# Optimization experiments

Measured on AMD Instinct MI355X. Metric: run time of the kernel, lower is better.

Reference implementation:

```python
import jax, jax.numpy as jnp
import numpy as np
from jax import lax

# Mamba hyperparams implied by Mamba(d_model=8, d_state=16, d_conv=4, expand=2)
D_MODEL, D_STATE, D_CONV, EXPAND = 8, 16, 4, 2
D_INNER = EXPAND * D_MODEL          # 16
DT_RANK = -(-D_MODEL // 16)          # ceil(8/16) = 1
BATCH, SEQ_LEN, NUM_CLASSES = 1024, 250, 12


def silu(v):
    return v * jax.nn.sigmoid(v)


def setup_inputs() -> dict:
    key = jax.random.key(0)
    ks = jax.random.split(key, 12)
    s = 0.05
    return {
        "x": jax.random.normal(ks[0], (BATCH, D_MODEL, SEQ_LEN), jnp.float32),
        "in_proj_w": jax.random.normal(ks[1], (2 * D_INNER, D_MODEL), jnp.float32) * s,
        "conv_w": jax.random.normal(ks[2], (D_INNER, D_CONV), jnp.float32) * s,
        "conv_b": jax.random.normal(ks[3], (D_INNER,), jnp.float32) * s,
        "x_proj_w": jax.random.normal(ks[4], (DT_RANK + 2 * D_STATE, D_INNER), jnp.float32) * s,
        "dt_proj_w": jax.random.normal(ks[5], (D_INNER, DT_RANK), jnp.float32) * s,
        "dt_proj_b": jax.random.normal(ks[6], (D_INNER,), jnp.float32) * s,
        "A_log": jnp.log(jnp.tile(jnp.arange(1, D_STATE + 1, dtype=jnp.float32), (D_INNER, 1))),
        "D": jnp.ones((D_INNER,), jnp.float32),
        "out_proj_w": jax.random.normal(ks[7], (D_MODEL, D_INNER), jnp.float32) * s,
        "fc_w": jax.random.normal(ks[8], (NUM_CLASSES, D_MODEL * SEQ_LEN), jnp.float32) * s,
        "fc_b": jax.random.normal(ks[9], (NUM_CLASSES,), jnp.float32) * s,
    }


def reference(x, in_proj_w, conv_w, conv_b, x_proj_w, dt_proj_w, dt_proj_b,
              A_log, D, out_proj_w, fc_w, fc_b):
    B = x.shape[0]
    xt = jnp.transpose(x, (0, 2, 1))                       # (B, L, d_model)
    xz = xt @ in_proj_w.T                                  # (B, L, 2*d_inner)
    x_in, z = xz[..., :D_INNER], xz[..., D_INNER:]

    # causal depthwise conv1d along time, kernel d_conv, padding d_conv-1, crop to L
    xp = jnp.pad(x_in, ((0, 0), (D_CONV - 1, 0), (0, 0)))  # (B, L+3, d_inner)
    acc = conv_b
    for k in range(D_CONV):  # small fixed kernel loop
        acc = acc + conv_w[:, k] * xp[:, k:k + SEQ_LEN, :]
    u = silu(acc)                                          # (B, L, d_inner)

    x_dbl = u @ x_proj_w.T                                 # (B, L, dt_rank+2*d_state)
    dt = x_dbl[..., :DT_RANK]
    Bm = x_dbl[..., DT_RANK:DT_RANK + D_STATE]             # (B, L, d_state)
    Cm = x_dbl[..., DT_RANK + D_STATE:]                    # (B, L, d_state)
    delta = jax.nn.softplus(dt @ dt_proj_w.T + dt_proj_b)  # (B, L, d_inner)

    A = -jnp.exp(A_log)                                    # (d_inner, d_state)
    dA = jnp.exp(delta[..., None] * A)                     # (B, L, d_inner, d_state)
    dBu = delta[..., None] * Bm[:, :, None, :] * u[..., None]

    def step(h, inp):
        dA_t, dBu_t, C_t = inp
        h = dA_t * h + dBu_t                               # (B, d_inner, d_state)
        y_t = jnp.einsum('bds,bs->bd', h, C_t)
        return h, y_t

    h0 = jnp.zeros((B, D_INNER, D_STATE), x.dtype)
    _, ys = lax.scan(step, h0, (jnp.moveaxis(dA, 1, 0),
                                jnp.moveaxis(dBu, 1, 0),
                                jnp.moveaxis(Cm, 1, 0)))
    y = jnp.moveaxis(ys, 0, 1) + u * D                     # (B, L, d_inner)
    y = y * silu(z)
    out = y @ out_proj_w.T                                 # (B, L, d_model)

    flat = out.reshape(B, D_MODEL * SEQ_LEN)
    return flat @ fc_w.T + fc_b                            # (B, num_classes)
```

## Files before the change

### kernel.cpp

```cpp
#include <hip/hip_runtime.h>
#include <hip/hip_fp16.h>
#include <math.h>

#define SEQ 250
#define ST  252
#define NCLS 12

typedef __attribute__((ext_vector_type(4))) _Float16 half4v;
typedef __attribute__((ext_vector_type(4))) float    float4v;

template<int CTRL>
__device__ __forceinline__ float dpp_add(float v) {
    int t = __builtin_amdgcn_update_dpp(0, __float_as_int(v), CTRL, 0xF, 0xF, true);
    return v + __int_as_float(t);
}

__device__ __forceinline__ __half2 f_as_h2(float f) {
    union { float f; __half2 h; } u; u.f = f; return u.h;
}
__device__ __forceinline__ float h2_as_f(__half2 h) {
    union { __half2 h; float f; } u; u.h = h; return u.f;
}

__global__ __launch_bounds__(512)
void mamba_cls_kernel(
    const float* __restrict__ x,
    const float* __restrict__ in_proj_w,
    const float* __restrict__ conv_w,
    const float* __restrict__ conv_b,
    const float* __restrict__ x_proj_w,
    const float* __restrict__ dt_proj_w,
    const float* __restrict__ dt_proj_b,
    const float* __restrict__ A_log,
    const float* __restrict__ Dp,
    const float* __restrict__ out_proj_w,
    const float* __restrict__ fc_w,
    const float* __restrict__ fc_b,
    float* __restrict__ out)
{
    __shared__ __align__(16) __half2 s_bc [2][16 * ST];
    __shared__ __align__(16) __half2 s_dlu[2][16 * ST];
    __shared__ __align__(16) __half  s_sz [2][16 * ST];

    const int tid  = threadIdx.x;
    const int p    = tid >> 8;
    const int tid8 = tid & 255;
    const int b0   = blockIdx.x * 2;

    {
        float4* s_xf4 = (float4*)s_dlu[0];
        const float4* __restrict__ xb4 =
            (const float4*)(x + (size_t)b0 * (8 * SEQ));
        for (int i = tid; i < 1000; i += 512) s_xf4[i] = xb4[i];
    }
    __syncthreads();

    {
        float* s_f  = (float*)s_bc[p];
        const float* s_xf = (const float*)s_dlu[0] + p * (8 * SEQ);
        const int d  = tid8 & 15;
        const int t0 = tid8 >> 4;
        float w1[8], w2[8];
        #pragma unroll
        for (int m = 0; m < 8; ++m) {
            w1[m] = in_proj_w[d * 8 + m];
            w2[m] = in_proj_w[(16 + d) * 8 + m];
        }
        #pragma unroll
        for (int i = 0; i < 16; ++i) {
            int t = t0 + i * 16;
            if (t < SEQ) {
                float acc = 0.f, z = 0.f;
                #pragma unroll
                for (int m = 0; m < 8; ++m) {
                    float xv = s_xf[m * SEQ + t];
                    acc = fmaf(w1[m], xv, acc);
                    z   = fmaf(w2[m], xv, z);
                }
                s_f[d * ST + t] = acc;
                s_sz[p][d * ST + t] = __float2half(z / (1.f + __expf(-z)));
            }
        }
    }
    __syncthreads();

    {
        const float* s_f = (const float*)s_bc[p];
        const int d  = tid8 & 15;
        const int t0 = tid8 >> 4;
        float cw[4];
        #pragma unroll
        for (int k = 0; k < 4; ++k) cw[k] = conv_w[d * 4 + k];
        const float cb = conv_b[d];
        #pragma unroll
        for (int i = 0; i < 16; ++i) {
            int t = t0 + i * 16;
            if (t < SEQ) {
                float acc = cb;
                #pragma unroll
                for (int k = 0; k < 4; ++k) {
                    int tt = t + k - 3;
                    if (tt >= 0) acc = fmaf(cw[k], s_f[d * ST + tt], acc);
                }
                float sg = 1.f / (1.f + __expf(-acc));
                s_dlu[p][d * ST + t].y = __float2half(acc * sg);
            }
        }
    }
    __syncthreads();

    {
        const int wave = tid8 >> 6;
        const int l    = tid8 & 63;
        const int rowc = l & 15;
        const int kg   = l >> 4;

        half4v wB, wC, wD;
        #pragma unroll
        for (int i = 0; i < 4; ++i) {
            wB[i] = (_Float16)x_proj_w[(1  + rowc) * 16 + 4 * kg + i];
            wC[i] = (_Float16)x_proj_w[(17 + rowc) * 16 + 4 * kg + i];
            wD[i] = (_Float16)x_proj_w[4 * kg + i];
        }
        const float dtw_c = dt_proj_w[rowc];
        const float dtb_c = dt_proj_b[rowc];
        const float4v zero4 = {0.f, 0.f, 0.f, 0.f};
        const unsigned int* __restrict__ dlu_w = (const unsigned int*)s_dlu[p];

        for (int tile = wave; tile < 16; tile += 4) {
            const int t0 = tile * 16;
            unsigned int w0 = dlu_w[(4 * kg + 0) * ST + t0 + rowc];
            unsigned int w1 = dlu_w[(4 * kg + 1) * ST + t0 + rowc];
            unsigned int w2 = dlu_w[(4 * kg + 2) * ST + t0 + rowc];
            unsigned int w3 = dlu_w[(4 * kg + 3) * ST + t0 + rowc];
            union { unsigned int u[2]; half4v h; } A;
            A.u[0] = (w0 >> 16) | (w1 & 0xFFFF0000u);
            A.u[1] = (w2 >> 16) | (w3 & 0xFFFF0000u);

            float4v dB = __builtin_amdgcn_mfma_f32_16x16x16f16(A.h, wB, zero4, 0, 0, 0);
            float4v dC = __builtin_amdgcn_mfma_f32_16x16x16f16(A.h, wC, zero4, 0, 0, 0);
            float4v dT = __builtin_amdgcn_mfma_f32_16x16x16f16(A.h, wD, zero4, 0, 0, 0);

            const int tb = t0 + kg * 4;
            if (tb <= 248) {
                __half2 h0 = __floats2half2_rn(dB[0], dC[0]);
                __half2 h1 = __floats2half2_rn(dB[1], dC[1]);
                __half2 h2 = __floats2half2_rn(dB[2], dC[2]);
                __half2 h3 = __floats2half2_rn(dB[3], dC[3]);
                float4 wv;
                wv.x = h2_as_f(h0); wv.y = h2_as_f(h1);
                wv.z = h2_as_f(h2); wv.w = h2_as_f(h3);
                *reinterpret_cast<float4*>(s_bc[p] + rowc * ST + tb) = wv;
            }
            #pragma unroll
            for (int r = 0; r < 4; ++r) {
                int t = tb + r;
                if (t < SEQ) {
                    float v  = fmaf(dT[r], dtw_c, dtb_c);
                    float dl = (v > 20.f) ? v : __logf(1.f + __expf(v));
                    s_dlu[p][rowc * ST + t].x = __float2half(dl);
                }
            }
        }
    }
    __syncthreads();

    if (tid < 256) {
        const int sp   = tid >> 7;
        const int i7   = tid & 127;
        const int d    = i7 >> 3;
        const int s2   = i7 & 7;
        const float A2a = -__expf(A_log[d * 16 + s2])     * 1.4426950408889634f;
        const float A2b = -__expf(A_log[d * 16 + s2 + 8]) * 1.4426950408889634f;
        const float Dd  = Dp[d];
        const __half2* __restrict__ dlu_p = s_dlu[sp] + d * ST;
        const __half2* __restrict__ bca_p = s_bc [sp] + s2 * ST;
        const __half2* __restrict__ bcb_p = s_bc [sp] + (s2 + 8) * ST;
        const __half*  __restrict__ sz_p  = (const __half*)s_sz[sp] + d * ST;
        float* __restrict__ y_p = (float*)s_dlu[sp] + d * ST;
        float ha = 0.f, hb = 0.f;
        for (int t = 0; t < 248; t += 8) {
            float4 du_a = *reinterpret_cast<const float4*>(dlu_p + t);
            float4 du_b = *reinterpret_cast<const float4*>(dlu_p + t + 4);
            float4 ba_a = *reinterpret_cast<const float4*>(bca_p + t);
            float4 ba_b = *reinterpret_cast<const float4*>(bca_p + t + 4);
            float4 bb_a = *reinterpret_cast<const float4*>(bcb_p + t);
            float4 bb_b = *reinterpret_cast<const float4*>(bcb_p + t + 4);
            float2 sza  = *reinterpret_cast<const float2*>(sz_p + t);
            float2 szb  = *reinterpret_cast<const float2*>(sz_p + t + 4);

            float fdu[8] = {du_a.x, du_a.y, du_a.z, du_a.w,
                            du_b.x, du_b.y, du_b.z, du_b.w};
            float fba[8] = {ba_a.x, ba_a.y, ba_a.z, ba_a.w,
                            ba_b.x, ba_b.y, ba_b.z, ba_b.w};
            float fbb[8] = {bb_a.x, bb_a.y, bb_a.z, bb_a.w,
                            bb_b.x, bb_b.y, bb_b.z, bb_b.w};
            float2 s0 = __half22float2(f_as_h2(sza.x));
            float2 s1 = __half22float2(f_as_h2(sza.y));
            float2 s2f = __half22float2(f_as_h2(szb.x));
            float2 s3 = __half22float2(f_as_h2(szb.y));
            float fsz[8] = {s0.x, s0.y, s1.x, s1.y, s2f.x, s2f.y, s3.x, s3.y};

            float yv[8];
            #pragma unroll
            for (int tt = 0; tt < 8; ++tt) {
                float2 du  = __half22float2(f_as_h2(fdu[tt]));
                float2 bca = __half22float2(f_as_h2(fba[tt]));
                float2 bcb = __half22float2(f_as_h2(fbb[tt]));
                float dlu = du.x * du.y;
                ha = fmaf(exp2f(du.x * A2a), ha, dlu * bca.x);
                hb = fmaf(exp2f(du.x * A2b), hb, dlu * bcb.x);
                float r = fmaf(hb, bcb.y, ha * bca.y);
                r = dpp_add<0xB1>(r);
                r = dpp_add<0x4E>(r);
                r = dpp_add<0x141>(r);
                yv[tt] = fmaf(du.y, Dd, r) * fsz[tt];
            }
            if (s2 == 0) {
                float4 y4;
                y4.x = yv[0]; y4.y = yv[1]; y4.z = yv[2]; y4.w = yv[3];
                *reinterpret_cast<float4*>(y_p + t) = y4;
                y4.x = yv[4]; y4.y = yv[5]; y4.z = yv[6]; y4.w = yv[7];
                *reinterpret_cast<float4*>(y_p + t + 4) = y4;
            }
        }
        {
            float2 duv2 = *reinterpret_cast<const float2*>(dlu_p + 248);
            float2 bca2 = *reinterpret_cast<const float2*>(bca_p + 248);
            float2 bcb2 = *reinterpret_cast<const float2*>(bcb_p + 248);
            float2 szf  = __half22float2(*reinterpret_cast<const __half2*>(sz_p + 248));
            float fdu[2] = {duv2.x, duv2.y};
            float fba[2] = {bca2.x, bca2.y};
            float fbb[2] = {bcb2.x, bcb2.y};
            float fsz[2] = {szf.x, szf.y};
            float yv[2];
            #pragma unroll
            for (int tt = 0; tt < 2; ++tt) {
                float2 du  = __half22float2(f_as_h2(fdu[tt]));
                float2 bca = __half22float2(f_as_h2(fba[tt]));
                float2 bcb = __half22float2(f_as_h2(fbb[tt]));
                float dlu = du.x * du.y;
                ha = fmaf(exp2f(du.x * A2a), ha, dlu * bca.x);
                hb = fmaf(exp2f(du.x * A2b), hb, dlu * bcb.x);
                float r = fmaf(hb, bcb.y, ha * bca.y);
                r = dpp_add<0xB1>(r);
                r = dpp_add<0x4E>(r);
                r = dpp_add<0x141>(r);
                yv[tt] = fmaf(du.y, Dd, r) * fsz[tt];
            }
            if (s2 == 0) {
                float2 y2; y2.x = yv[0]; y2.y = yv[1];
                *reinterpret_cast<float2*>(y_p + 248) = y2;
            }
        }
    }
    __syncthreads();

    {
        float* s_f  = (float*)s_bc[p];
        const float* s_yf = (const float*)s_dlu[p];
        const int j = tid8 & 7;
        float w[16];
        #pragma unroll
        for (int d2 = 0; d2 < 16; ++d2) w[d2] = out_proj_w[j * 16 + d2];
        for (int t0 = (tid8 >> 3) * 4; t0 < SEQ; t0 += 128) {
            float a0 = 0.f, a1 = 0.f, a2 = 0.f, a3 = 0.f;
            #pragma unroll
            for (int d2 = 0; d2 < 16; ++d2) {
                float4 y4 = *reinterpret_cast<const float4*>(s_yf + d2 * ST + t0);
                a0 = fmaf(w[d2], y4.x, a0);
                a1 = fmaf(w[d2], y4.y, a1);
                a2 = fmaf(w[d2], y4.z, a2);
                a3 = fmaf(w[d2], y4.w, a3);
            }
            s_f[(t0 + 0) * 8 + j] = a0;
            s_f[(t0 + 1) * 8 + j] = a1;
            if (t0 + 2 < SEQ) s_f[(t0 + 2) * 8 + j] = a2;
            if (t0 + 3 < SEQ) s_f[(t0 + 3) * 8 + j] = a3;
        }
    }
    __syncthreads();

    {
        float* s_yf = (float*)s_dlu[p];
        float p_[NCLS];
        #pragma unroll
        for (int c = 0; c < NCLS; ++c) p_[c] = 0.f;
        const float4* fw4 = (const float4*)fc_w;
        const float4* sf4 = (const float4*)s_bc[p];
        for (int q = tid8; q < 500; q += 256) {
            float4 f = sf4[q];
            #pragma unroll
            for (int c = 0; c < NCLS; ++c) {
                float4 wv = fw4[c * 500 + q];
                p_[c] += f.x * wv.x + f.y * wv.y + f.z * wv.z + f.w * wv.w;
            }
        }
        #pragma unroll
        for (int c = 0; c < NCLS; ++c) {
            float v = p_[c];
            v = dpp_add<0xB1>(v);
            v = dpp_add<0x4E>(v);
            v = dpp_add<0x141>(v);
            v = dpp_add<0x140>(v);
            v += __shfl_xor(v, 16);
            v += __shfl_xor(v, 32);
            p_[c] = v;
        }
        const int wave = tid8 >> 6;
        const int lane = tid8 & 63;
        __syncthreads();
        if (lane == 0) {
            #pragma unroll
            for (int c = 0; c < NCLS; ++c) s_yf[wave * NCLS + c] = p_[c];
        }
        __syncthreads();
        if (tid8 < NCLS) {
            float v = s_yf[tid8] + s_yf[NCLS + tid8] + s_yf[2 * NCLS + tid8] +
                      s_yf[3 * NCLS + tid8] + fc_b[tid8];
            out[(size_t)(b0 + p) * NCLS + tid8] = v;
        }
    }
}

extern "C" void kernel_launch(void* const* d_in, const int* in_sizes, int n_in,
                              void* d_out, int out_size, void* d_ws, size_t ws_size,
                              hipStream_t stream) {
    const float* x          = (const float*)d_in[0];
    const float* in_proj_w  = (const float*)d_in[1];
    const float* conv_w     = (const float*)d_in[2];
    const float* conv_b     = (const float*)d_in[3];
    const float* x_proj_w   = (const float*)d_in[4];
    const float* dt_proj_w  = (const float*)d_in[5];
    const float* dt_proj_b  = (const float*)d_in[6];
    const float* A_log      = (const float*)d_in[7];
    const float* Dp         = (const float*)d_in[8];
    const float* out_proj_w = (const float*)d_in[9];
    const float* fc_w       = (const float*)d_in[10];
    const float* fc_b       = (const float*)d_in[11];
    float* out = (float*)d_out;

    const int batch = in_sizes[0] / (8 * SEQ);
    mamba_cls_kernel<<<batch / 2, 512, 0, stream>>>(
        x, in_proj_w, conv_w, conv_b, x_proj_w, dt_proj_w, dt_proj_b,
        A_log, Dp, out_proj_w, fc_w, fc_b, out);
}
```

Before: 53.42 us.

## Split selective scan into two time halves with state carry-over correction

The sequential scan over 250 steps previously used only 256 of 512 threads. Now the first half of threads scans steps 0-127 while the second half scans 128-249 from a zero state. It records the cumulative delta sum and partial output packed in fp16. A third pass then adds the carried-in state contribution, C·h127·exp(A·cumsum delta), for the second half. This halves the serial dependency chain but adds a sync, an extra correction pass, and fp16 rounding of cumulative sums and of the mid state, which risks accuracy loss.

```diff
diff --git a/kernel.cpp b/kernel.cpp
--- a/kernel.cpp
+++ b/kernel.cpp
@@ -41,6 +41,7 @@
     __shared__ __align__(16) __half2 s_bc [2][16 * ST];
     __shared__ __align__(16) __half2 s_dlu[2][16 * ST];
     __shared__ __align__(16) __half  s_sz [2][16 * ST];
+    __shared__ __half s_h127[2][256];
 
     const int tid  = threadIdx.x;
     const int p    = tid >> 8;
@@ -165,92 +166,175 @@
     }
     __syncthreads();
 
-    if (tid < 256) {
-        const int sp   = tid >> 7;
-        const int i7   = tid & 127;
-        const int d    = i7 >> 3;
-        const int s2   = i7 & 7;
+    {
+        const int sp = (tid >> 7) & 1;
+        const int i7 = tid & 127;
+        const int d  = i7 >> 3;
+        const int s2 = i7 & 7;
         const float A2a = -__expf(A_log[d * 16 + s2])     * 1.4426950408889634f;
         const float A2b = -__expf(A_log[d * 16 + s2 + 8]) * 1.4426950408889634f;
         const float Dd  = Dp[d];
         const __half2* __restrict__ dlu_p = s_dlu[sp] + d * ST;
         const __half2* __restrict__ bca_p = s_bc [sp] + s2 * ST;
         const __half2* __restrict__ bcb_p = s_bc [sp] + (s2 + 8) * ST;
-        const __half*  __restrict__ sz_p  = (const __half*)s_sz[sp] + d * ST;
         float* __restrict__ y_p = (float*)s_dlu[sp] + d * ST;
         float ha = 0.f, hb = 0.f;
-        for (int t = 0; t < 248; t += 8) {
-            float4 du_a = *reinterpret_cast<const float4*>(dlu_p + t);
-            float4 du_b = *reinterpret_cast<const float4*>(dlu_p + t + 4);
-            float4 ba_a = *reinterpret_cast<const float4*>(bca_p + t);
-            float4 ba_b = *reinterpret_cast<const float4*>(bca_p + t + 4);
-            float4 bb_a = *reinterpret_cast<const float4*>(bcb_p + t);
-            float4 bb_b = *reinterpret_cast<const float4*>(bcb_p + t + 4);
-            float2 sza  = *reinterpret_cast<const float2*>(sz_p + t);
-            float2 szb  = *reinterpret_cast<const float2*>(sz_p + t + 4);
-
-            float fdu[8] = {du_a.x, du_a.y, du_a.z, du_a.w,
-                            du_b.x, du_b.y, du_b.z, du_b.w};
-            float fba[8] = {ba_a.x, ba_a.y, ba_a.z, ba_a.w,
-                            ba_b.x, ba_b.y, ba_b.z, ba_b.w};
-            float fbb[8] = {bb_a.x, bb_a.y, bb_a.z, bb_a.w,
-                            bb_b.x, bb_b.y, bb_b.z, bb_b.w};
-            float2 s0 = __half22float2(f_as_h2(sza.x));
-            float2 s1 = __half22float2(f_as_h2(sza.y));
-            float2 s2f = __half22float2(f_as_h2(szb.x));
-            float2 s3 = __half22float2(f_as_h2(szb.y));
-            float fsz[8] = {s0.x, s0.y, s1.x, s1.y, s2f.x, s2f.y, s3.x, s3.y};
-
-            float yv[8];
-            #pragma unroll
-            for (int tt = 0; tt < 8; ++tt) {
-                float2 du  = __half22float2(f_as_h2(fdu[tt]));
-                float2 bca = __half22float2(f_as_h2(fba[tt]));
-                float2 bcb = __half22float2(f_as_h2(fbb[tt]));
-                float dlu = du.x * du.y;
-                ha = fmaf(exp2f(du.x * A2a), ha, dlu * bca.x);
-                hb = fmaf(exp2f(du.x * A2b), hb, dlu * bcb.x);
-                float r = fmaf(hb, bcb.y, ha * bca.y);
-                r = dpp_add<0xB1>(r);
-                r = dpp_add<0x4E>(r);
-                r = dpp_add<0x141>(r);
-                yv[tt] = fmaf(du.y, Dd, r) * fsz[tt];
-            }
-            if (s2 == 0) {
-                float4 y4;
-                y4.x = yv[0]; y4.y = yv[1]; y4.z = yv[2]; y4.w = yv[3];
-                *reinterpret_cast<float4*>(y_p + t) = y4;
-                y4.x = yv[4]; y4.y = yv[5]; y4.z = yv[6]; y4.w = yv[7];
-                *reinterpret_cast<float4*>(y_p + t + 4) = y4;
-            }
-        }
-        {
-            float2 duv2 = *reinterpret_cast<const float2*>(dlu_p + 248);
-            float2 bca2 = *reinterpret_cast<const float2*>(bca_p + 248);
-            float2 bcb2 = *reinterpret_cast<const float2*>(bcb_p + 248);
-            float2 szf  = __half22float2(*reinterpret_cast<const __half2*>(sz_p + 248));
-            float fdu[2] = {duv2.x, duv2.y};
-            float fba[2] = {bca2.x, bca2.y};
-            float fbb[2] = {bcb2.x, bcb2.y};
-            float fsz[2] = {szf.x, szf.y};
-            float yv[2];
-            #pragma unroll
-            for (int tt = 0; tt < 2; ++tt) {
-                float2 du  = __half22float2(f_as_h2(fdu[tt]));
-                float2 bca = __half22float2(f_as_h2(fba[tt]));
-                float2 bcb = __half22float2(f_as_h2(fbb[tt]));
-                float dlu = du.x * du.y;
-                ha = fmaf(exp2f(du.x * A2a), ha, dlu * bca.x);
-                hb = fmaf(exp2f(du.x * A2b), hb, dlu * bcb.x);
-                float r = fmaf(hb, bcb.y, ha * bca.y);
-                r = dpp_add<0xB1>(r);
-                r = dpp_add<0x4E>(r);
-                r = dpp_add<0x141>(r);
-                yv[tt] = fmaf(du.y, Dd, r) * fsz[tt];
-            }
-            if (s2 == 0) {
-                float2 y2; y2.x = yv[0]; y2.y = yv[1];
-                *reinterpret_cast<float2*>(y_p + 248) = y2;
+
+        if (tid < 256) {
+            const __half* __restrict__ sz_p = (const __half*)s_sz[sp] + d * ST;
+            for (int t = 0; t < 128; t += 8) {
+                float4 du_a = *reinterpret_cast<const float4*>(dlu_p + t);
+                float4 du_b = *reinterpret_cast<const float4*>(dlu_p + t + 4);
+                float4 ba_a = *reinterpret_cast<const float4*>(bca_p + t);
+                float4 ba_b = *reinterpret_cast<const float4*>(bca_p + t + 4);
+                float4 bb_a = *reinterpret_cast<const float4*>(bcb_p + t);
+                float4 bb_b = *reinterpret_cast<const float4*>(bcb_p + t + 4);
+                float2 sza  = *reinterpret_cast<const float2*>(sz_p + t);
+                float2 szb  = *reinterpret_cast<const float2*>(sz_p + t + 4);
+
+                float fdu[8] = {du_a.x, du_a.y, du_a.z, du_a.w,
+                                du_b.x, du_b.y, du_b.z, du_b.w};
+                float fba[8] = {ba_a.x, ba_a.y, ba_a.z, ba_a.w,
+                                ba_b.x, ba_b.y, ba_b.z, ba_b.w};
+                float fbb[8] = {bb_a.x, bb_a.y, bb_a.z, bb_a.w,
+                                bb_b.x, bb_b.y, bb_b.z, bb_b.w};
+                float2 s0 = __half22float2(f_as_h2(sza.x));
+                float2 s1 = __half22float2(f_as_h2(sza.y));
+                float2 s2f = __half22float2(f_as_h2(szb.x));
+                float2 s3 = __half22float2(f_as_h2(szb.y));
+                float fsz[8] = {s0.x, s0.y, s1.x, s1.y, s2f.x, s2f.y, s3.x, s3.y};
+
+                float yv[8];
+                #pragma unroll
+                for (int q = 0; q < 8; ++q) {
+                    float2 du  = __half22float2(f_as_h2(fdu[q]));
+                    float2 bca = __half22float2(f_as_h2(fba[q]));
+                    float2 bcb = __half22float2(f_as_h2(fbb[q]));
+                    float dlu = du.x * du.y;
+                    ha = fmaf(exp2f(du.x * A2a), ha, dlu * bca.x);
+                    hb = fmaf(exp2f(du.x * A2b), hb, dlu * bcb.x);
+                    float r = fmaf(hb, bcb.y, ha * bca.y);
+                    r = dpp_add<0xB1>(r);
+                    r = dpp_add<0x4E>(r);
+                    r = dpp_add<0x141>(r);
+                    yv[q] = fmaf(du.y, Dd, r) * fsz[q];
+                }
+                if (s2 == 0) {
+                    float4 y4;
+                    y4.x = yv[0]; y4.y = yv[1]; y4.z = yv[2]; y4.w = yv[3];
+                    *reinterpret_cast<float4*>(y_p + t) = y4;
+                    y4.x = yv[4]; y4.y = yv[5]; y4.z = yv[6]; y4.w = yv[7];
+                    *reinterpret_cast<float4*>(y_p + t + 4) = y4;
+                }
+            }
+            s_h127[sp][d * 16 + s2]     = __float2half(ha);
+            s_h127[sp][d * 16 + s2 + 8] = __float2half(hb);
+        } else {
+            float Ssum = 0.f;
+            for (int t = 128; t < 248; t += 8) {
+                float4 du_a = *reinterpret_cast<const float4*>(dlu_p + t);
+                float4 du_b = *reinterpret_cast<const float4*>(dlu_p + t + 4);
+                float4 ba_a = *reinterpret_cast<const float4*>(bca_p + t);
+                float4 ba_b = *reinterpret_cast<const float4*>(bca_p + t + 4);
+                float4 bb_a = *reinterpret_cast<const float4*>(bcb_p + t);
+                float4 bb_b = *reinterpret_cast<const float4*>(bcb_p + t + 4);
+
+                float fdu[8] = {du_a.x, du_a.y, du_a.z, du_a.w,
+                                du_b.x, du_b.y, du_b.z, du_b.w};
+                float fba[8] = {ba_a.x, ba_a.y, ba_a.z, ba_a.w,
+                                ba_b.x, ba_b.y, ba_b.z, ba_b.w};
+                float fbb[8] = {bb_a.x, bb_a.y, bb_a.z, bb_a.w,
+                                bb_b.x, bb_b.y, bb_b.z, bb_b.w};
+                float wpk[8];
+                #pragma unroll
+                for (int q = 0; q < 8; ++q) {
+                    float2 du  = __half22float2(f_as_h2(fdu[q]));
+                    float2 bca = __half22float2(f_as_h2(fba[q]));
+                    float2 bcb = __half22float2(f_as_h2(fbb[q]));
+                    Ssum += du.x;
+                    float dlu = du.x * du.y;
+                    ha = fmaf(exp2f(du.x * A2a), ha, dlu * bca.x);
+                    hb = fmaf(exp2f(du.x * A2b), hb, dlu * bcb.x);
+                    float r = fmaf(hb, bcb.y, ha * bca.y);
+                    r = dpp_add<0xB1>(r);
+                    r = dpp_add<0x4E>(r);
+                    r = dpp_add<0x141>(r);
+                    float ypart = fmaf(du.y, Dd, r);
+                    wpk[q] = h2_as_f(__floats2half2_rn(Ssum, ypart));
+                }
+                if (s2 == 0) {
+                    float4 y4;
+                    y4.x = wpk[0]; y4.y = wpk[1]; y4.z = wpk[2]; y4.w = wpk[3];
+                    *reinterpret_cast<float4*>(y_p + t) = y4;
+                    y4.x = wpk[4]; y4.y = wpk[5]; y4.z = wpk[6]; y4.w = wpk[7];
+                    *reinterpret_cast<float4*>(y_p + t + 4) = y4;
+                }
+            }
+            {
+                float2 duv2 = *reinterpret_cast<const float2*>(dlu_p + 248);
+                float2 bca2 = *reinterpret_cast<const float2*>(bca_p + 248);
+                float2 bcb2 = *reinterpret_cast<const float2*>(bcb_p + 248);
+                float fdu[2] = {duv2.x, duv2.y};
+                float fba[2] = {bca2.x, bca2.y};
+                float fbb[2] = {bcb2.x, bcb2.y};
+                float wpk[2];
+                #pragma unroll
+                for (int q = 0; q < 2; ++q) {
+                    float2 du  = __half22float2(f_as_h2(fdu[q]));
+                    float2 bca = __half22float2(f_as_h2(fba[q]));
+                    float2 bcb = __half22float2(f_as_h2(fbb[q]));
+                    Ssum += du.x;
+                    float dlu = du.x * du.y;
+                    ha = fmaf(exp2f(du.x * A2a), ha, dlu * bca.x);
+                    hb = fmaf(exp2f(du.x * A2b), hb, dlu * bcb.x);
+                    float r = fmaf(hb, bcb.y, ha * bca.y);
+                    r = dpp_add<0xB1>(r);
+                    r = dpp_add<0x4E>(r);
+                    r = dpp_add<0x141>(r);
+                    float ypart = fmaf(du.y, Dd, r);
+                    wpk[q] = h2_as_f(__floats2half2_rn(Ssum, ypart));
+                }
+                if (s2 == 0) {
+                    float2 y2; y2.x = wpk[0]; y2.y = wpk[1];
+                    *reinterpret_cast<float2*>(y_p + 248) = y2;
+                }
+            }
+        }
+    }
+    __syncthreads();
+
+    {
+        const int d = tid8 >> 4;
+        const int s = tid8 & 15;
+        const float A2 = -__expf(A_log[d * 16 + s]) * 1.4426950408889634f;
+        const float hmid = __half2float(s_h127[p][d * 16 + s]);
+        float* __restrict__ y_row = (float*)s_dlu[p] + d * ST;
+        const __half2* __restrict__ bc_row = s_bc[p] + s * ST;
+        const __half*  __restrict__ sz_row = (const __half*)s_sz[p] + d * ST;
+        for (int t = 128; t < 250; t += 2) {
+            float2 w2 = *reinterpret_cast<const float2*>(y_row + t);
+            float2 c2 = *reinterpret_cast<const float2*>(bc_row + t);
+            float  szw = *reinterpret_cast<const float*>(sz_row + t);
+            float2 szv = __half22float2(f_as_h2(szw));
+
+            float2 w0 = __half22float2(f_as_h2(w2.x));
+            float2 w1 = __half22float2(f_as_h2(w2.y));
+            float  C0 = __half22float2(f_as_h2(c2.x)).y;
+            float  C1 = __half22float2(f_as_h2(c2.y)).y;
+
+            float corr0 = C0 * hmid * exp2f(A2 * w0.x);
+            corr0 = dpp_add<0xB1>(corr0);
+            corr0 = dpp_add<0x4E>(corr0);
+            corr0 = dpp_add<0x141>(corr0);
+            corr0 = dpp_add<0x140>(corr0);
+            float corr1 = C1 * hmid * exp2f(A2 * w1.x);
+            corr1 = dpp_add<0xB1>(corr1);
+            corr1 = dpp_add<0x4E>(corr1);
+            corr1 = dpp_add<0x141>(corr1);
+            corr1 = dpp_add<0x140>(corr1);
+            if (s == 0) {
+                y_row[t]     = (w0.y + corr0) * szv.x;
+                y_row[t + 1] = (w1.y + corr1) * szv.y;
             }
         }
     }
```

After: 70.89 us. +32.7%, slower.

## Fuse in_proj and causal conv per thread with contiguous time chunks

Applied to the files above, without the earlier changes.

Each thread now handles a contiguous 16-step time chunk for one channel rather than strided steps. This lets the in_proj output feed the depthwise conv straight from registers, with a 3-step halo recomputed. The separate shared-memory staging pass and one block barrier go away, and shared-memory loads and stores become vectorized float4 accesses. In exchange the kernel uses more registers, and the halo projection is recomputed for every chunk.

```diff
diff --git a/kernel.cpp b/kernel.cpp
--- a/kernel.cpp
+++ b/kernel.cpp
@@ -48,7 +48,7 @@
     const int b0   = blockIdx.x * 2;
 
     {
-        float4* s_xf4 = (float4*)s_dlu[0];
+        float4* s_xf4 = (float4*)s_bc[0];
         const float4* __restrict__ xb4 =
             (const float4*)(x + (size_t)b0 * (8 * SEQ));
         for (int i = tid; i < 1000; i += 512) s_xf4[i] = xb4[i];
@@ -56,54 +56,91 @@
     __syncthreads();
 
     {
-        float* s_f  = (float*)s_bc[p];
-        const float* s_xf = (const float*)s_dlu[0] + p * (8 * SEQ);
+        const float* s_xf = (const float*)s_bc[0] + p * (8 * SEQ);
         const int d  = tid8 & 15;
-        const int t0 = tid8 >> 4;
-        float w1[8], w2[8];
+        const int c  = tid8 >> 4;
+        const int t0 = c * 16;
+        float w1[8], w2[8], cw[4];
         #pragma unroll
         for (int m = 0; m < 8; ++m) {
             w1[m] = in_proj_w[d * 8 + m];
             w2[m] = in_proj_w[(16 + d) * 8 + m];
         }
         #pragma unroll
-        for (int i = 0; i < 16; ++i) {
-            int t = t0 + i * 16;
-            if (t < SEQ) {
+        for (int k = 0; k < 4; ++k) cw[k] = conv_w[d * 4 + k];
+        const float cb = conv_b[d];
+
+        float xm3 = 0.f, xm2 = 0.f, xm1 = 0.f;
+        if (t0 > 0) {
+            #pragma unroll
+            for (int m = 0; m < 8; ++m) {
+                float a = s_xf[m * SEQ + t0 - 3];
+                float b = s_xf[m * SEQ + t0 - 2];
+                float cc = s_xf[m * SEQ + t0 - 1];
+                xm3 = fmaf(w1[m], a, xm3);
+                xm2 = fmaf(w1[m], b, xm2);
+                xm1 = fmaf(w1[m], cc, xm1);
+            }
+        }
+
+        float xin[16];
+        __half szh[16];
+        #pragma unroll
+        for (int g = 0; g < 4; ++g) {
+            float4 xv[8];
+            #pragma unroll
+            for (int m = 0; m < 8; ++m)
+                xv[m] = *reinterpret_cast<const float4*>(s_xf + m * SEQ + t0 + g * 4);
+            #pragma unroll
+            for (int j = 0; j < 4; ++j) {
                 float acc = 0.f, z = 0.f;
                 #pragma unroll
                 for (int m = 0; m < 8; ++m) {
-                    float xv = s_xf[m * SEQ + t];
-                    acc = fmaf(w1[m], xv, acc);
-                    z   = fmaf(w2[m], xv, z);
+                    float xvj = ((const float*)&xv[m])[j];
+                    acc = fmaf(w1[m], xvj, acc);
+                    z   = fmaf(w2[m], xvj, z);
                 }
-                s_f[d * ST + t] = acc;
-                s_sz[p][d * ST + t] = __float2half(z / (1.f + __expf(-z)));
-            }
-        }
-    }
-    __syncthreads();
-
-    {
-        const float* s_f = (const float*)s_bc[p];
-        const int d  = tid8 & 15;
-        const int t0 = tid8 >> 4;
-        float cw[4];
-        #pragma unroll
-        for (int k = 0; k < 4; ++k) cw[k] = conv_w[d * 4 + k];
-        const float cb = conv_b[d];
+                xin[g * 4 + j] = acc;
+                szh[g * 4 + j] = __float2half(z / (1.f + __expf(-z)));
+            }
+        }
+
+        {
+            __half* szp = (__half*)s_sz[p] + d * ST + t0;
+            if (c < 15) {
+                *reinterpret_cast<float4*>(szp)     = *reinterpret_cast<float4*>(&szh[0]);
+                *reinterpret_cast<float4*>(szp + 8) = *reinterpret_cast<float4*>(&szh[8]);
+            } else {
+                *reinterpret_cast<float4*>(szp)     = *reinterpret_cast<float4*>(&szh[0]);
+                *reinterpret_cast<float*>(szp + 8)  = *reinterpret_cast<float*>(&szh[8]);
+            }
+        }
+
+        float uw[16];
         #pragma unroll
         for (int i = 0; i < 16; ++i) {
-            int t = t0 + i * 16;
-            if (t < SEQ) {
-                float acc = cb;
+            float a = (i >= 3) ? xin[i - 3] : (i == 0 ? xm3 : (i == 1 ? xm2 : xm1));
+            float b = (i >= 2) ? xin[i - 2] : (i == 0 ? xm2 : xm1);
+            float cc = (i >= 1) ? xin[i - 1] : xm1;
+            float acc = cb;
+            acc = fmaf(cw[0], a,  acc);
+            acc = fmaf(cw[1], b,  acc);
+            acc = fmaf(cw[2], cc, acc);
+            acc = fmaf(cw[3], xin[i], acc);
+            float sg = 1.f / (1.f + __expf(-acc));
+            uw[i] = __uint_as_float(((unsigned)__half_as_ushort(__float2half(acc * sg))) << 16);
+        }
+        {
+            float* dlup = (float*)(s_dlu[p] + d * ST + t0);
+            if (c < 15) {
                 #pragma unroll
-                for (int k = 0; k < 4; ++k) {
-                    int tt = t + k - 3;
-                    if (tt >= 0) acc = fmaf(cw[k], s_f[d * ST + tt], acc);
-                }
-                float sg = 1.f / (1.f + __expf(-acc));
-                s_dlu[p][d * ST + t].y = __float2half(acc * sg);
+                for (int g = 0; g < 4; ++g)
+                    *reinterpret_cast<float4*>(dlup + g * 4) =
+                        *reinterpret_cast<float4*>(&uw[g * 4]);
+            } else {
+                *reinterpret_cast<float4*>(dlup)     = *reinterpret_cast<float4*>(&uw[0]);
+                *reinterpret_cast<float4*>(dlup + 4) = *reinterpret_cast<float4*>(&uw[4]);
+                *reinterpret_cast<float2*>(dlup + 8) = *reinterpret_cast<float2*>(&uw[8]);
             }
         }
     }
```

New measurement: 68.39 us. 28.0% more time.
